# Kernel optimization log

Hardware: AMD Instinct MI355X
Metric: run time of the kernel (lower is better)

## Reference

```python
import jax, jax.numpy as jnp
import numpy as np

B, T, F = 64, 128, 9            # batch, seq_len, n_feature_fields
N_FEATURES = 32000              # vocab for embedding (N_FEATURES-1 rows) and fc head
EMB = 8
H = 16                          # lstm hidden size
IN0 = (F - 1) * EMB + 1         # lstm layer-0 input size = 65


def setup_inputs() -> dict:
    key = jax.random.key(0)
    ks = jax.random.split(key, 16)
    # x: first F-1 columns are integer-valued categorical indices, last column numeric
    cat = jax.random.randint(ks[0], (B, T, F - 1), 0, N_FEATURES - 1).astype(jnp.float32)
    num = jax.random.normal(ks[1], (B, T, 1), dtype=jnp.float32)
    x = jnp.concatenate([cat, num], axis=-1)
    h0 = jnp.zeros((2, B, H), dtype=jnp.float32)
    c0 = jnp.zeros((2, B, H), dtype=jnp.float32)
    emb = jax.random.normal(ks[2], (N_FEATURES - 1, EMB), dtype=jnp.float32)
    s0 = 1.0 / np.sqrt(IN0)
    s1 = 1.0 / np.sqrt(H)
    W_ih0 = jax.random.normal(ks[3], (4 * H, IN0), dtype=jnp.float32) * s0
    W_hh0 = jax.random.normal(ks[4], (4 * H, H), dtype=jnp.float32) * s1
    b_ih0 = jax.random.normal(ks[5], (4 * H,), dtype=jnp.float32) * 0.1
    b_hh0 = jax.random.normal(ks[6], (4 * H,), dtype=jnp.float32) * 0.1
    W_ih1 = jax.random.normal(ks[7], (4 * H, H), dtype=jnp.float32) * s1
    W_hh1 = jax.random.normal(ks[8], (4 * H, H), dtype=jnp.float32) * s1
    b_ih1 = jax.random.normal(ks[9], (4 * H,), dtype=jnp.float32) * 0.1
    b_hh1 = jax.random.normal(ks[10], (4 * H,), dtype=jnp.float32) * 0.1
    fc_w = jax.random.normal(ks[11], (N_FEATURES, H), dtype=jnp.float32) * (1.0 / np.sqrt(H))
    fc_b = jax.random.normal(ks[12], (N_FEATURES,), dtype=jnp.float32) * 0.1
    return {"x": x, "h0": h0, "c0": c0, "emb": emb,
            "W_ih0": W_ih0, "W_hh0": W_hh0, "b_ih0": b_ih0, "b_hh0": b_hh0,
            "W_ih1": W_ih1, "W_hh1": W_hh1, "b_ih1": b_ih1, "b_hh1": b_hh1,
            "fc_w": fc_w, "fc_b": fc_b}


def _lstm_layer(xs, h0, c0, Wih, Whh, bih, bhh):
    # xs: [B, T, I]; PyTorch gate order: i, f, g, o
    xp = jnp.einsum('bti,gi->btg', xs, Wih) + (bih + bhh)  # [B, T, 4H]
    xp = jnp.swapaxes(xp, 0, 1)  # [T, B, 4H]

    def step(carry, xt):
        h, c = carry
        g = xt + h @ Whh.T
        i, f, gg, o = jnp.split(g, 4, axis=-1)
        c = jax.nn.sigmoid(f) * c + jax.nn.sigmoid(i) * jnp.tanh(gg)
        h = jax.nn.sigmoid(o) * jnp.tanh(c)
        return (h, c), h

    (hT, cT), ys = jax.lax.scan(step, (h0, c0), xp)
    return jnp.swapaxes(ys, 0, 1), hT, cT


def reference(x, h0, c0, emb, W_ih0, W_hh0, b_ih0, b_hh0,
              W_ih1, W_hh1, b_ih1, b_hh1, fc_w, fc_b):
    cat = x[:, :, :-1].astype(jnp.int32)          # [B, T, F-1]
    num = x[:, :, -1:]                            # [B, T, 1]
    e = emb[cat].reshape(x.shape[0], x.shape[1], -1)  # [B, T, (F-1)*EMB]
    inp = jnp.concatenate([e, num], axis=-1)      # [B, T, IN0]
    y0, h0T, c0T = _lstm_layer(inp, h0[0], c0[0], W_ih0, W_hh0, b_ih0, b_hh0)
    y1, h1T, c1T = _lstm_layer(y0, h0[1], c0[1], W_ih1, W_hh1, b_ih1, b_hh1)
    logits = jnp.einsum('bth,vh->btv', y1, fc_w) + fc_b  # [B, T, N_FEATURES]
    hN = jnp.stack([h0T, h1T], axis=0)
    cN = jnp.stack([c0T, c1T], axis=0)
    return logits, hN, cN
```

## Files before the change

### kernel.cpp

```cpp
#include <hip/hip_runtime.h>
#include <math.h>

#define BB 64
#define TT 128
#define HH 16
#define GG 64
#define IN0_ 65
#define VV 32000
#define NROWS (BB*TT)
#define RSTRIDE 68

typedef float f32x4 __attribute__((ext_vector_type(4)));

__device__ __forceinline__ float sigf(float x) {
    return 1.0f / (1.0f + __expf(-x));
}
__device__ __forceinline__ float tanhfast(float x) {
    return 1.0f - 2.0f / (__expf(2.0f * x) + 1.0f);
}

__global__ __launch_bounds__(256) void fused_front(const float* __restrict__ x,
                           const float* __restrict__ emb,
                           const float* __restrict__ Wih0, const float* __restrict__ bih0,
                           const float* __restrict__ bhh0,
                           const float* __restrict__ h0in, const float* __restrict__ c0in,
                           const float* __restrict__ Whh0,
                           const float* __restrict__ Wih1, const float* __restrict__ Whh1,
                           const float* __restrict__ bih1, const float* __restrict__ bhh1,
                           float* __restrict__ y1, float* __restrict__ outTail) {
    __shared__ float insh[TT * RSTRIDE];
    __shared__ float wsh[GG * IN0_];
    const int b   = blockIdx.x;
    const int tid = threadIdx.x;
    const int wave = tid >> 6, g = tid & 63;
    const float* xb = x + (size_t)b * TT * 9;

    for (int i = tid; i < GG * IN0_ / 4; i += 256) {
        float4 wv = *reinterpret_cast<const float4*>(Wih0 + i * 4);
        wsh[i*4+0] = wv.x; wsh[i*4+1] = wv.y; wsh[i*4+2] = wv.z; wsh[i*4+3] = wv.w;
    }
    #pragma unroll
    for (int it = 0; it < 8; ++it) {
        int q = tid + it * 256;
        int p = q >> 1, half = q & 1;
        int r = p >> 3, f = p & 7;
        int idx = (int)xb[r * 9 + f];
        const float* er = emb + (size_t)idx * 8 + half * 4;
        float4 e = *reinterpret_cast<const float4*>(er);
        float* d = &insh[r * RSTRIDE + f * 8 + half * 4];
        d[0] = e.x; d[1] = e.y; d[2] = e.z; d[3] = e.w;
    }
    if (tid < TT) insh[tid * RSTRIDE + 64] = xb[tid * 9 + 8];
    __syncthreads();

    {
        float wreg[IN0_];
        #pragma unroll
        for (int k = 0; k < IN0_; ++k) wreg[k] = wsh[g * IN0_ + k];
        const float bias0 = bih0[g] + bhh0[g];
        for (int r = 0; r < 32; ++r) {
            const int row = wave * 32 + r;
            const float* ir = &insh[row * RSTRIDE];
            float a0 = bias0, a1 = 0.0f, a2 = 0.0f, a3 = 0.0f;
            #pragma unroll
            for (int k4 = 0; k4 < 16; ++k4) {
                f32x4 v = *reinterpret_cast<const f32x4*>(ir + k4 * 4);
                float p0 = v.x * wreg[k4*4+0] + v.y * wreg[k4*4+1]
                         + v.z * wreg[k4*4+2] + v.w * wreg[k4*4+3];
                if ((k4 & 3) == 0) a0 += p0;
                else if ((k4 & 3) == 1) a1 += p0;
                else if ((k4 & 3) == 2) a2 += p0;
                else a3 += p0;
            }
            float acc = (a0 + a1) + (a2 + a3) + ir[64] * wreg[64];
            insh[row * RSTRIDE + g] = acc;
        }
    }
    __syncthreads();

    if (tid >= 64) return;

    const int j = g & 15;
    float w0[HH], wi1[HH], w1[HH];
    #pragma unroll
    for (int k = 0; k < HH; ++k) {
        w0[k]  = Whh0[g * HH + k];
        wi1[k] = Wih1[g * HH + k];
        w1[k]  = Whh1[g * HH + k];
    }
    const float bias1 = bih1[g] + bhh1[g];

    float h0v = h0in[b * HH + j];
    float h1v = h0in[BB * HH + b * HH + j];
    float c0v = c0in[b * HH + j];
    float c1v = c0in[BB * HH + b * HH + j];

    {
        float aa = insh[g], ab = 0.0f;
        #pragma unroll
        for (int k = 0; k < 8; ++k) {
            aa += __shfl(h0v, k) * w0[k];
            ab += __shfl(h0v, k + 8) * w0[k + 8];
        }
        float acc = aa + ab;
        float iv = __shfl(acc, j), fv = __shfl(acc, j + 16);
        float gv = __shfl(acc, j + 32), ov = __shfl(acc, j + 48);
        c0v = sigf(fv) * c0v + sigf(iv) * tanhfast(gv);
        h0v = sigf(ov) * tanhfast(c0v);
    }

    for (int t = 0; t < TT - 1; ++t) {
        float xpn = insh[(t + 1) * RSTRIDE + g];
        float a1a = bias1, a1b = 0.0f, a1c = 0.0f, a1d = 0.0f;
        float a0a = 0.0f,  a0b = 0.0f;
        #pragma unroll
        for (int k = 0; k < 8; ++k) {
            float h0k  = __shfl(h0v, k);
            float h0k8 = __shfl(h0v, k + 8);
            float h1k  = __shfl(h1v, k);
            float h1k8 = __shfl(h1v, k + 8);
            a1a += h0k  * wi1[k];
            a1b += h0k8 * wi1[k + 8];
            a1c += h1k  * w1[k];
            a1d += h1k8 * w1[k + 8];
            a0a += h0k  * w0[k];
            a0b += h0k8 * w0[k + 8];
        }
        float acc1 = (a1a + a1b) + (a1c + a1d);
        float acc0 = xpn + a0a + a0b;
        float iv1 = __shfl(acc1, j), fv1 = __shfl(acc1, j + 16);
        float gv1 = __shfl(acc1, j + 32), ov1 = __shfl(acc1, j + 48);
        float iv0 = __shfl(acc0, j), fv0 = __shfl(acc0, j + 16);
        float gv0 = __shfl(acc0, j + 32), ov0 = __shfl(acc0, j + 48);
        c1v = sigf(fv1) * c1v + sigf(iv1) * tanhfast(gv1);
        h1v = sigf(ov1) * tanhfast(c1v);
        c0v = sigf(fv0) * c0v + sigf(iv0) * tanhfast(gv0);
        h0v = sigf(ov0) * tanhfast(c0v);
        if (g < HH) y1[(size_t)(b * TT + t) * HH + g] = h1v;
    }

    {
        float a1a = bias1, a1b = 0.0f, a1c = 0.0f, a1d = 0.0f;
        #pragma unroll
        for (int k = 0; k < 8; ++k) {
            float h0k  = __shfl(h0v, k);
            float h0k8 = __shfl(h0v, k + 8);
            float h1k  = __shfl(h1v, k);
            float h1k8 = __shfl(h1v, k + 8);
            a1a += h0k  * wi1[k];
            a1b += h0k8 * wi1[k + 8];
            a1c += h1k  * w1[k];
            a1d += h1k8 * w1[k + 8];
        }
        float acc1 = (a1a + a1b) + (a1c + a1d);
        float iv1 = __shfl(acc1, j), fv1 = __shfl(acc1, j + 16);
        float gv1 = __shfl(acc1, j + 32), ov1 = __shfl(acc1, j + 48);
        c1v = sigf(fv1) * c1v + sigf(iv1) * tanhfast(gv1);
        h1v = sigf(ov1) * tanhfast(c1v);
        if (g < HH) y1[(size_t)(b * TT + TT - 1) * HH + g] = h1v;
    }

    if (g < HH) {
        outTail[b * HH + g]               = h0v;
        outTail[BB * HH + b * HH + g]     = h1v;
        outTail[2 * BB * HH + b * HH + g] = c0v;
        outTail[3 * BB * HH + b * HH + g] = c1v;
    }
}

__global__ __launch_bounds__(256) void fc_kernel(const float* __restrict__ y1,
                          const float* __restrict__ fcw, const float* __restrict__ fcb,
                          float* __restrict__ out) {
    const int tid  = threadIdx.x;
    const int v0   = blockIdx.y * 1024 + tid * 4;
    const int row0 = blockIdx.x * 32;

    if (v0 >= VV) return;

    float w[4][HH];
    #pragma unroll
    for (int jj = 0; jj < 4; ++jj) {
        const float4* wp = reinterpret_cast<const float4*>(fcw + (size_t)(v0 + jj) * HH);
        float4 a = wp[0], b = wp[1], c = wp[2], d = wp[3];
        w[jj][0]=a.x; w[jj][1]=a.y; w[jj][2]=a.z; w[jj][3]=a.w;
        w[jj][4]=b.x; w[jj][5]=b.y; w[jj][6]=b.z; w[jj][7]=b.w;
        w[jj][8]=c.x; w[jj][9]=c.y; w[jj][10]=c.z; w[jj][11]=c.w;
        w[jj][12]=d.x; w[jj][13]=d.y; w[jj][14]=d.z; w[jj][15]=d.w;
    }
    const float4 bias = *reinterpret_cast<const float4*>(fcb + v0);

    const f32x4* yrow = reinterpret_cast<const f32x4*>(y1 + (size_t)row0 * HH);

    float* orow = out + (size_t)row0 * VV + v0;
    #pragma unroll 4
    for (int r = 0; r < 32; ++r) {
        f32x4 y0 = yrow[r * 4 + 0];
        f32x4 y1v = yrow[r * 4 + 1];
        f32x4 y2 = yrow[r * 4 + 2];
        f32x4 y3 = yrow[r * 4 + 3];
        float a0 = bias.x, a1 = bias.y, a2 = bias.z, a3 = bias.w;
        #pragma unroll
        for (int jj = 0; jj < 4; ++jj) {
            float* wj = w[jj];
            float acc = y0.x*wj[0] + y0.y*wj[1] + y0.z*wj[2] + y0.w*wj[3]
                      + y1v.x*wj[4] + y1v.y*wj[5] + y1v.z*wj[6] + y1v.w*wj[7]
                      + y2.x*wj[8] + y2.y*wj[9] + y2.z*wj[10] + y2.w*wj[11]
                      + y3.x*wj[12] + y3.y*wj[13] + y3.z*wj[14] + y3.w*wj[15];
            if (jj == 0) a0 += acc;
            else if (jj == 1) a1 += acc;
            else if (jj == 2) a2 += acc;
            else a3 += acc;
        }
        f32x4 o;
        o.x = a0; o.y = a1; o.z = a2; o.w = a3;
        __builtin_nontemporal_store(o, reinterpret_cast<f32x4*>(orow));
        orow += VV;
    }
}

extern "C" void kernel_launch(void* const* d_in, const int* in_sizes, int n_in,
                              void* d_out, int out_size, void* d_ws, size_t ws_size,
                              hipStream_t stream) {
    const float* x    = (const float*)d_in[0];
    const float* h0   = (const float*)d_in[1];
    const float* c0   = (const float*)d_in[2];
    const float* emb  = (const float*)d_in[3];
    const float* Wih0 = (const float*)d_in[4];
    const float* Whh0 = (const float*)d_in[5];
    const float* bih0 = (const float*)d_in[6];
    const float* bhh0 = (const float*)d_in[7];
    const float* Wih1 = (const float*)d_in[8];
    const float* Whh1 = (const float*)d_in[9];
    const float* bih1 = (const float*)d_in[10];
    const float* bhh1 = (const float*)d_in[11];
    const float* fcw  = (const float*)d_in[12];
    const float* fcb  = (const float*)d_in[13];

    float* out = (float*)d_out;
    float* y1  = (float*)d_ws;
    float* outTail = out + (size_t)NROWS * VV;

    fused_front<<<BB, 256, 0, stream>>>(x, emb, Wih0, bih0, bhh0, h0, c0,
                                        Whh0, Wih1, Whh1, bih1, bhh1, y1, outTail);
    fc_kernel<<<dim3(NROWS / 32, 32), 256, 0, stream>>>(y1, fcw, fcb, out);
}
```

Baseline: 304.6 us.

## Fuse LSTM recurrence and FC head into one kernel with flag-based streaming

```diff
diff --git a/kernel.cpp b/kernel.cpp
--- a/kernel.cpp
+++ b/kernel.cpp
@@ -19,45 +19,45 @@
     return 1.0f - 2.0f / (__expf(2.0f * x) + 1.0f);
 }
 
-__global__ __launch_bounds__(256) void fused_front(const float* __restrict__ x,
-                           const float* __restrict__ emb,
-                           const float* __restrict__ Wih0, const float* __restrict__ bih0,
-                           const float* __restrict__ bhh0,
-                           const float* __restrict__ h0in, const float* __restrict__ c0in,
-                           const float* __restrict__ Whh0,
-                           const float* __restrict__ Wih1, const float* __restrict__ Whh1,
-                           const float* __restrict__ bih1, const float* __restrict__ bhh1,
-                           float* __restrict__ y1, float* __restrict__ outTail) {
+__global__ __launch_bounds__(256) void fused_all(
+    const float* __restrict__ x, const float* __restrict__ emb,
+    const float* __restrict__ Wih0, const float* __restrict__ bih0,
+    const float* __restrict__ bhh0,
+    const float* __restrict__ h0in, const float* __restrict__ c0in,
+    const float* __restrict__ Whh0, const float* __restrict__ Wih1,
+    const float* __restrict__ Whh1, const float* __restrict__ bih1,
+    const float* __restrict__ bhh1,
+    const float* __restrict__ fcw, const float* __restrict__ fcb,
+    float* __restrict__ y1, float* __restrict__ outTail,
+    unsigned int* __restrict__ flags, float* __restrict__ out)
+{
     __shared__ float insh[TT * RSTRIDE];
-    __shared__ float wsh[GG * IN0_];
-    const int b   = blockIdx.x;
     const int tid = threadIdx.x;
-    const int wave = tid >> 6, g = tid & 63;
-    const float* xb = x + (size_t)b * TT * 9;
-
-    for (int i = tid; i < GG * IN0_ / 4; i += 256) {
-        float4 wv = *reinterpret_cast<const float4*>(Wih0 + i * 4);
-        wsh[i*4+0] = wv.x; wsh[i*4+1] = wv.y; wsh[i*4+2] = wv.z; wsh[i*4+3] = wv.w;
-    }
-    #pragma unroll
-    for (int it = 0; it < 8; ++it) {
-        int q = tid + it * 256;
-        int p = q >> 1, half = q & 1;
-        int r = p >> 3, f = p & 7;
-        int idx = (int)xb[r * 9 + f];
-        const float* er = emb + (size_t)idx * 8 + half * 4;
-        float4 e = *reinterpret_cast<const float4*>(er);
-        float* d = &insh[r * RSTRIDE + f * 8 + half * 4];
-        d[0] = e.x; d[1] = e.y; d[2] = e.z; d[3] = e.w;
-    }
-    if (tid < TT) insh[tid * RSTRIDE + 64] = xb[tid * 9 + 8];
-    __syncthreads();
-
-    {
+
+    if (blockIdx.x < BB) {
+        const int b = blockIdx.x;
+        const int wave = tid >> 6, g = tid & 63;
+        const float* xb = x + (size_t)b * TT * 9;
+
+        #pragma unroll
+        for (int it = 0; it < 8; ++it) {
+            int q = tid + it * 256;
+            int p = q >> 1, half = q & 1;
+            int r = p >> 3, f = p & 7;
+            int idx = (int)xb[r * 9 + f];
+            const float* er = emb + (size_t)idx * 8 + half * 4;
+            float4 e = *reinterpret_cast<const float4*>(er);
+            float* d = &insh[r * RSTRIDE + f * 8 + half * 4];
+            d[0] = e.x; d[1] = e.y; d[2] = e.z; d[3] = e.w;
+        }
+        if (tid < TT) insh[tid * RSTRIDE + 64] = xb[tid * 9 + 8];
+
         float wreg[IN0_];
         #pragma unroll
-        for (int k = 0; k < IN0_; ++k) wreg[k] = wsh[g * IN0_ + k];
+        for (int k = 0; k < IN0_; ++k) wreg[k] = Wih0[g * IN0_ + k];
         const float bias0 = bih0[g] + bhh0[g];
+        __syncthreads();
+
         for (int r = 0; r < 32; ++r) {
             const int row = wave * 32 + r;
             const float* ir = &insh[row * RSTRIDE];
@@ -75,146 +75,159 @@
             float acc = (a0 + a1) + (a2 + a3) + ir[64] * wreg[64];
             insh[row * RSTRIDE + g] = acc;
         }
-    }
-    __syncthreads();
-
-    if (tid >= 64) return;
-
-    const int j = g & 15;
-    float w0[HH], wi1[HH], w1[HH];
-    #pragma unroll
-    for (int k = 0; k < HH; ++k) {
-        w0[k]  = Whh0[g * HH + k];
-        wi1[k] = Wih1[g * HH + k];
-        w1[k]  = Whh1[g * HH + k];
-    }
-    const float bias1 = bih1[g] + bhh1[g];
-
-    float h0v = h0in[b * HH + j];
-    float h1v = h0in[BB * HH + b * HH + j];
-    float c0v = c0in[b * HH + j];
-    float c1v = c0in[BB * HH + b * HH + j];
-
-    {
-        float aa = insh[g], ab = 0.0f;
-        #pragma unroll
-        for (int k = 0; k < 8; ++k) {
-            aa += __shfl(h0v, k) * w0[k];
-            ab += __shfl(h0v, k + 8) * w0[k + 8];
-        }
-        float acc = aa + ab;
-        float iv = __shfl(acc, j), fv = __shfl(acc, j + 16);
-        float gv = __shfl(acc, j + 32), ov = __shfl(acc, j + 48);
-        c0v = sigf(fv) * c0v + sigf(iv) * tanhfast(gv);
-        h0v = sigf(ov) * tanhfast(c0v);
-    }
-
-    for (int t = 0; t < TT - 1; ++t) {
-        float xpn = insh[(t + 1) * RSTRIDE + g];
-        float a1a = bias1, a1b = 0.0f, a1c = 0.0f, a1d = 0.0f;
-        float a0a = 0.0f,  a0b = 0.0f;
-        #pragma unroll
-        for (int k = 0; k < 8; ++k) {
-            float h0k  = __shfl(h0v, k);
-            float h0k8 = __shfl(h0v, k + 8);
-            float h1k  = __shfl(h1v, k);
-            float h1k8 = __shfl(h1v, k + 8);
-            a1a += h0k  * wi1[k];
-            a1b += h0k8 * wi1[k + 8];
-            a1c += h1k  * w1[k];
-            a1d += h1k8 * w1[k + 8];
-            a0a += h0k  * w0[k];
-            a0b += h0k8 * w0[k + 8];
-        }
-        float acc1 = (a1a + a1b) + (a1c + a1d);
-        float acc0 = xpn + a0a + a0b;
-        float iv1 = __shfl(acc1, j), fv1 = __shfl(acc1, j + 16);
-        float gv1 = __shfl(acc1, j + 32), ov1 = __shfl(acc1, j + 48);
-        float iv0 = __shfl(acc0, j), fv0 = __shfl(acc0, j + 16);
-        float gv0 = __shfl(acc0, j + 32), ov0 = __shfl(acc0, j + 48);
-        c1v = sigf(fv1) * c1v + sigf(iv1) * tanhfast(gv1);
-        h1v = sigf(ov1) * tanhfast(c1v);
-        c0v = sigf(fv0) * c0v + sigf(iv0) * tanhfast(gv0);
-        h0v = sigf(ov0) * tanhfast(c0v);
-        if (g < HH) y1[(size_t)(b * TT + t) * HH + g] = h1v;
-    }
-
-    {
-        float a1a = bias1, a1b = 0.0f, a1c = 0.0f, a1d = 0.0f;
-        #pragma unroll
-        for (int k = 0; k < 8; ++k) {
-            float h0k  = __shfl(h0v, k);
-            float h0k8 = __shfl(h0v, k + 8);
-            float h1k  = __shfl(h1v, k);
-            float h1k8 = __shfl(h1v, k + 8);
-            a1a += h0k  * wi1[k];
-            a1b += h0k8 * wi1[k + 8];
-            a1c += h1k  * w1[k];
-            a1d += h1k8 * w1[k + 8];
-        }
-        float acc1 = (a1a + a1b) + (a1c + a1d);
-        float iv1 = __shfl(acc1, j), fv1 = __shfl(acc1, j + 16);
-        float gv1 = __shfl(acc1, j + 32), ov1 = __shfl(acc1, j + 48);
-        c1v = sigf(fv1) * c1v + sigf(iv1) * tanhfast(gv1);
-        h1v = sigf(ov1) * tanhfast(c1v);
-        if (g < HH) y1[(size_t)(b * TT + TT - 1) * HH + g] = h1v;
-    }
-
-    if (g < HH) {
-        outTail[b * HH + g]               = h0v;
-        outTail[BB * HH + b * HH + g]     = h1v;
-        outTail[2 * BB * HH + b * HH + g] = c0v;
-        outTail[3 * BB * HH + b * HH + g] = c1v;
-    }
-}
-
-__global__ __launch_bounds__(256) void fc_kernel(const float* __restrict__ y1,
-                          const float* __restrict__ fcw, const float* __restrict__ fcb,
-                          float* __restrict__ out) {
-    const int tid  = threadIdx.x;
-    const int v0   = blockIdx.y * 1024 + tid * 4;
-    const int row0 = blockIdx.x * 32;
-
-    if (v0 >= VV) return;
-
-    float w[4][HH];
-    #pragma unroll
-    for (int jj = 0; jj < 4; ++jj) {
-        const float4* wp = reinterpret_cast<const float4*>(fcw + (size_t)(v0 + jj) * HH);
-        float4 a = wp[0], b = wp[1], c = wp[2], d = wp[3];
-        w[jj][0]=a.x; w[jj][1]=a.y; w[jj][2]=a.z; w[jj][3]=a.w;
-        w[jj][4]=b.x; w[jj][5]=b.y; w[jj][6]=b.z; w[jj][7]=b.w;
-        w[jj][8]=c.x; w[jj][9]=c.y; w[jj][10]=c.z; w[jj][11]=c.w;
-        w[jj][12]=d.x; w[jj][13]=d.y; w[jj][14]=d.z; w[jj][15]=d.w;
-    }
-    const float4 bias = *reinterpret_cast<const float4*>(fcb + v0);
-
-    const f32x4* yrow = reinterpret_cast<const f32x4*>(y1 + (size_t)row0 * HH);
-
-    float* orow = out + (size_t)row0 * VV + v0;
-    #pragma unroll 4
-    for (int r = 0; r < 32; ++r) {
-        f32x4 y0 = yrow[r * 4 + 0];
-        f32x4 y1v = yrow[r * 4 + 1];
-        f32x4 y2 = yrow[r * 4 + 2];
-        f32x4 y3 = yrow[r * 4 + 3];
-        float a0 = bias.x, a1 = bias.y, a2 = bias.z, a3 = bias.w;
+        __syncthreads();
+
+        if (tid >= 64) return;
+
+        const int j = g & 15;
+        float w0[HH], wi1[HH], w1[HH];
+        #pragma unroll
+        for (int k = 0; k < HH; ++k) {
+            w0[k]  = Whh0[g * HH + k];
+            wi1[k] = Wih1[g * HH + k];
+            w1[k]  = Whh1[g * HH + k];
+        }
+        const float bias1 = bih1[g] + bhh1[g];
+
+        float h0v = h0in[b * HH + j];
+        float h1v = h0in[BB * HH + b * HH + j];
+        float c0v = c0in[b * HH + j];
+        float c1v = c0in[BB * HH + b * HH + j];
+
+        {
+            float aa = insh[g], ab = 0.0f;
+            #pragma unroll
+            for (int k = 0; k < 8; ++k) {
+                aa += __shfl(h0v, k) * w0[k];
+                ab += __shfl(h0v, k + 8) * w0[k + 8];
+            }
+            float acc = aa + ab;
+            float iv = __shfl(acc, j), fv = __shfl(acc, j + 16);
+            float gv = __shfl(acc, j + 32), ov = __shfl(acc, j + 48);
+            c0v = sigf(fv) * c0v + sigf(iv) * tanhfast(gv);
+            h0v = sigf(ov) * tanhfast(c0v);
+        }
+
+        for (int t = 0; t < TT - 1; ++t) {
+            float xpn = insh[(t + 1) * RSTRIDE + g];
+            float a1a = bias1, a1b = 0.0f, a1c = 0.0f, a1d = 0.0f;
+            float a0a = 0.0f,  a0b = 0.0f;
+            #pragma unroll
+            for (int k = 0; k < 8; ++k) {
+                float h0k  = __shfl(h0v, k);
+                float h0k8 = __shfl(h0v, k + 8);
+                float h1k  = __shfl(h1v, k);
+                float h1k8 = __shfl(h1v, k + 8);
+                a1a += h0k  * wi1[k];
+                a1b += h0k8 * wi1[k + 8];
+                a1c += h1k  * w1[k];
+                a1d += h1k8 * w1[k + 8];
+                a0a += h0k  * w0[k];
+                a0b += h0k8 * w0[k + 8];
+            }
+            float acc1 = (a1a + a1b) + (a1c + a1d);
+            float acc0 = xpn + a0a + a0b;
+            float iv1 = __shfl(acc1, j), fv1 = __shfl(acc1, j + 16);
+            float gv1 = __shfl(acc1, j + 32), ov1 = __shfl(acc1, j + 48);
+            float iv0 = __shfl(acc0, j), fv0 = __shfl(acc0, j + 16);
+            float gv0 = __shfl(acc0, j + 32), ov0 = __shfl(acc0, j + 48);
+            c1v = sigf(fv1) * c1v + sigf(iv1) * tanhfast(gv1);
+            h1v = sigf(ov1) * tanhfast(c1v);
+            c0v = sigf(fv0) * c0v + sigf(iv0) * tanhfast(gv0);
+            h0v = sigf(ov0) * tanhfast(c0v);
+            if (g < HH) y1[(size_t)(b * TT + t) * HH + g] = h1v;
+            if (g == 0 && (t & 31) == 31)
+                __hip_atomic_store(&flags[b * 4 + (t >> 5)], 1u,
+                                   __ATOMIC_RELEASE, __HIP_MEMORY_SCOPE_AGENT);
+        }
+
+        {
+            float a1a = bias1, a1b = 0.0f, a1c = 0.0f, a1d = 0.0f;
+            #pragma unroll
+            for (int k = 0; k < 8; ++k) {
+                float h0k  = __shfl(h0v, k);
+                float h0k8 = __shfl(h0v, k + 8);
+                float h1k  = __shfl(h1v, k);
+                float h1k8 = __shfl(h1v, k + 8);
+                a1a += h0k  * wi1[k];
+                a1b += h0k8 * wi1[k + 8];
+                a1c += h1k  * w1[k];
+                a1d += h1k8 * w1[k + 8];
+            }
+            float acc1 = (a1a + a1b) + (a1c + a1d);
+            float iv1 = __shfl(acc1, j), fv1 = __shfl(acc1, j + 16);
+            float gv1 = __shfl(acc1, j + 32), ov1 = __shfl(acc1, j + 48);
+            c1v = sigf(fv1) * c1v + sigf(iv1) * tanhfast(gv1);
+            h1v = sigf(ov1) * tanhfast(c1v);
+            if (g < HH) y1[(size_t)(b * TT + TT - 1) * HH + g] = h1v;
+        }
+
+        if (g < HH) {
+            outTail[b * HH + g]               = h0v;
+            outTail[BB * HH + b * HH + g]     = h1v;
+            outTail[2 * BB * HH + b * HH + g] = c0v;
+            outTail[3 * BB * HH + b * HH + g] = c1v;
+        }
+        if (g == 0)
+            __hip_atomic_store(&flags[b * 4 + 3], 1u,
+                               __ATOMIC_RELEASE, __HIP_MEMORY_SCOPE_AGENT);
+    } else {
+        const int fcIdx = blockIdx.x - BB;
+        const int col   = fcIdx & 31;
+        const int band  = fcIdx >> 5;
+        const int c     = band >> 6;
+        const int bb    = band & 63;
+        const int row0  = bb * TT + c * 32;
+        const int v0    = col * 1024 + tid * 4;
+
+        if (tid == 0) {
+            while (__hip_atomic_load(&flags[bb * 4 + c],
+                                     __ATOMIC_ACQUIRE, __HIP_MEMORY_SCOPE_AGENT) == 0u)
+                __builtin_amdgcn_s_sleep(8);
+        }
+        __syncthreads();
+        if (v0 >= VV) return;
+
+        float w[4][HH];
         #pragma unroll
         for (int jj = 0; jj < 4; ++jj) {
-            float* wj = w[jj];
-            float acc = y0.x*wj[0] + y0.y*wj[1] + y0.z*wj[2] + y0.w*wj[3]
-                      + y1v.x*wj[4] + y1v.y*wj[5] + y1v.z*wj[6] + y1v.w*wj[7]
-                      + y2.x*wj[8] + y2.y*wj[9] + y2.z*wj[10] + y2.w*wj[11]
-                      + y3.x*wj[12] + y3.y*wj[13] + y3.z*wj[14] + y3.w*wj[15];
-            if (jj == 0) a0 += acc;
-            else if (jj == 1) a1 += acc;
-            else if (jj == 2) a2 += acc;
-            else a3 += acc;
-        }
-        f32x4 o;
-        o.x = a0; o.y = a1; o.z = a2; o.w = a3;
-        __builtin_nontemporal_store(o, reinterpret_cast<f32x4*>(orow));
-        orow += VV;
+            const float4* wp = reinterpret_cast<const float4*>(fcw + (size_t)(v0 + jj) * HH);
+            float4 a = wp[0], bq = wp[1], cq = wp[2], d = wp[3];
+            w[jj][0]=a.x; w[jj][1]=a.y; w[jj][2]=a.z; w[jj][3]=a.w;
+            w[jj][4]=bq.x; w[jj][5]=bq.y; w[jj][6]=bq.z; w[jj][7]=bq.w;
+            w[jj][8]=cq.x; w[jj][9]=cq.y; w[jj][10]=cq.z; w[jj][11]=cq.w;
+            w[jj][12]=d.x; w[jj][13]=d.y; w[jj][14]=d.z; w[jj][15]=d.w;
+        }
+        const float4 bias = *reinterpret_cast<const float4*>(fcb + v0);
+
+        const volatile f32x4* yrow =
+            reinterpret_cast<const volatile f32x4*>(y1 + (size_t)row0 * HH);
+
+        float* orow = out + (size_t)row0 * VV + v0;
+        #pragma unroll 4
+        for (int r = 0; r < 32; ++r) {
+            f32x4 y0 = yrow[r * 4 + 0];
+            f32x4 y1v = yrow[r * 4 + 1];
+            f32x4 y2 = yrow[r * 4 + 2];
+            f32x4 y3 = yrow[r * 4 + 3];
+            float a0 = bias.x, a1 = bias.y, a2 = bias.z, a3 = bias.w;
+            #pragma unroll
+            for (int jj = 0; jj < 4; ++jj) {
+                float* wj = w[jj];
+                float acc = y0.x*wj[0] + y0.y*wj[1] + y0.z*wj[2] + y0.w*wj[3]
+                          + y1v.x*wj[4] + y1v.y*wj[5] + y1v.z*wj[6] + y1v.w*wj[7]
+                          + y2.x*wj[8] + y2.y*wj[9] + y2.z*wj[10] + y2.w*wj[11]
+                          + y3.x*wj[12] + y3.y*wj[13] + y3.z*wj[14] + y3.w*wj[15];
+                if (jj == 0) a0 += acc;
+                else if (jj == 1) a1 += acc;
+                else if (jj == 2) a2 += acc;
+                else a3 += acc;
+            }
+            f32x4 o;
+            o.x = a0; o.y = a1; o.z = a2; o.w = a3;
+            __builtin_nontemporal_store(o, reinterpret_cast<f32x4*>(orow));
+            orow += VV;
+        }
     }
 }
 
@@ -237,10 +250,12 @@
     const float* fcb  = (const float*)d_in[13];
 
     float* out = (float*)d_out;
-    float* y1  = (float*)d_ws;
+    unsigned int* flags = (unsigned int*)d_ws;
+    float* y1 = (float*)((char*)d_ws + 1024);
     float* outTail = out + (size_t)NROWS * VV;
 
-    fused_front<<<BB, 256, 0, stream>>>(x, emb, Wih0, bih0, bhh0, h0, c0,
-                                        Whh0, Wih1, Whh1, bih1, bhh1, y1, outTail);
-    fc_kernel<<<dim3(NROWS / 32, 32), 256, 0, stream>>>(y1, fcw, fcb, out);
-}
+    hipMemsetAsync(flags, 0, 256 * sizeof(unsigned int), stream);
+    fused_all<<<BB + NROWS / 32 * 32, 256, 0, stream>>>(
+        x, emb, Wih0, bih0, bhh0, h0, c0, Whh0, Wih1, Whh1, bih1, bhh1,
+        fcw, fcb, y1, outTail, flags, out);
+}
```

After: 390.2 us. +28.1%, slower.
